# Kernel optimization log

Hardware: AMD Instinct MI355X
Metric: run time of the kernel (lower is better)

Reference implementation:

```python
import jax, jax.numpy as jnp
import numpy as np
import math

NBITS = (1, 2, 4, 8)
S, B, D, H, F = 1024, 8, 1024, 16, 4096
HD = D // H


def _quant(w, nbit):
    """Symmetric uniform weight quantization to `nbit` bits with STE."""
    if nbit == 1:
        q = jnp.sign(w) * jnp.mean(jnp.abs(w))
    else:
        qmax = float(2 ** (nbit - 1) - 1)
        scale = jnp.max(jnp.abs(w)) / qmax
        q = jnp.clip(jnp.round(w / scale), -qmax - 1.0, qmax) * scale
    # straight-through estimator: forward uses q, backward flows through w
    return w + jax.lax.stop_gradient(q - w)


def _layernorm(x, g, b, eps=1e-5):
    m = jnp.mean(x, axis=-1, keepdims=True)
    v = jnp.var(x, axis=-1, keepdims=True)
    return (x - m) * jax.lax.rsqrt(v + eps) * g + b


def _quant_attn(src, w_in, b_in, w_out, b_out, nbit):
    # src: [S,B,D]; w_in: [3D,D]; w_out: [D,D]
    w_in_q = _quant(w_in, nbit)
    w_out_q = _quant(w_out, nbit)
    qkv = jnp.einsum('sbd,ed->sbe', src, w_in_q) + b_in  # [S,B,3D]
    q, k, v = jnp.split(qkv, 3, axis=-1)
    q = q.reshape(S, B, H, HD)
    k = k.reshape(S, B, H, HD)
    v = v.reshape(S, B, H, HD)
    scores = jnp.einsum('sbhd,tbhd->bhst', q, k) * (1.0 / math.sqrt(HD))
    p = jax.nn.softmax(scores, axis=-1)  # [B,H,S,S]
    o = jnp.einsum('bhst,tbhd->sbhd', p, v).reshape(S, B, D)
    return jnp.einsum('sbd,ed->sbe', o, w_out_q) + b_out


def setup_inputs() -> dict:
    key = jax.random.key(0)
    ks = jax.random.split(key, 12)
    sc = 0.02
    return {
        'src': jax.random.normal(ks[0], (S, B, D), jnp.float32),
        'alpha': jax.random.normal(ks[1], (3, 4), jnp.float32),
        'in_proj_w': jax.random.normal(ks[2], (4, 3 * D, D), jnp.float32) * sc,
        'in_proj_b': jnp.zeros((4, 3 * D), jnp.float32),
        'out_proj_w': jax.random.normal(ks[3], (4, D, D), jnp.float32) * sc,
        'out_proj_b': jnp.zeros((4, D), jnp.float32),
        'w1': jax.random.normal(ks[4], (4, F, D), jnp.float32) * sc,
        'b1': jnp.zeros((4, F), jnp.float32),
        'w2': jax.random.normal(ks[5], (4, D, F), jnp.float32) * sc,
        'b2': jnp.zeros((4, D), jnp.float32),
        'g1': jnp.ones((D,), jnp.float32),
        'be1': jnp.zeros((D,), jnp.float32),
        'g2': jnp.ones((D,), jnp.float32),
        'be2': jnp.zeros((D,), jnp.float32),
    }


def reference(src, alpha, in_proj_w, in_proj_b, out_proj_w, out_proj_b,
              w1, b1, w2, b2, g1, be1, g2, be2):
    probs = jax.nn.softmax(alpha, axis=-1)  # [3,4]
    # softmax-weighted mixture of multi-bitwidth attention branches
    src2 = jnp.zeros_like(src)
    for i, nbit in enumerate(NBITS):
        src2 = src2 + probs[0, i] * _quant_attn(
            src, in_proj_w[i], in_proj_b[i], out_proj_w[i], out_proj_b[i], nbit)
    x = _layernorm(src + src2, g1, be1)
    # mixture of quantized linear1 branches, then GELU
    h = jnp.zeros((S, B, F), src.dtype)
    for i, nbit in enumerate(NBITS):
        h = h + probs[1, i] * (jnp.einsum('sbd,fd->sbf', x, _quant(w1[i], nbit)) + b1[i])
    h = jax.nn.gelu(h, approximate=False)
    # mixture of quantized linear2 branches
    y = jnp.zeros_like(x)
    for i, nbit in enumerate(NBITS):
        y = y + probs[2, i] * (jnp.einsum('sbf,df->sbd', h, _quant(w2[i], nbit)) + b2[i])
    return _layernorm(x + y, g2, be2)
```

## Files before the change

kernel.cpp:

```cpp
#include <hip/hip_runtime.h>
#include <hip/hip_bf16.h>

typedef __attribute__((ext_vector_type(8))) unsigned short u16x8;
typedef __attribute__((ext_vector_type(4))) unsigned short u16x4;
typedef __attribute__((ext_vector_type(4))) int            i32x4;
typedef __attribute__((ext_vector_type(8))) __bf16         bf16x8;
typedef __attribute__((ext_vector_type(4))) float          f32x4;

#define SS 1024
#define BB 8
#define DD 1024
#define HH 16
#define HDD 64
#define FF 4096
#define MM 8192

#define GL16(g, l) __builtin_amdgcn_global_load_lds( \
    (__attribute__((address_space(1))) const void*)(g), \
    (__attribute__((address_space(3))) void*)(l), 16, 0, 0)

__device__ __forceinline__ float bf2f(unsigned short u) {
    return __uint_as_float(((unsigned int)u) << 16);
}
__device__ __forceinline__ unsigned short f2bf(float f) {
    return __builtin_bit_cast(unsigned short, (__bf16)f);
}
__device__ __forceinline__ float quantv(float w, float som, float qm) {
    if (qm == 0.f) {
        float sgn = (w > 0.f) ? 1.f : ((w < 0.f) ? -1.f : 0.f);
        return sgn * som;
    }
    if (som == 0.f) return 0.f;
    float q = rintf(w / som);
    q = fminf(fmaxf(q, -qm - 1.f), qm);
    return q * som;
}

__global__ __launch_bounds__(256) void k_stats(const float* __restrict__ w_in, const float* __restrict__ w_out,
                                               const float* __restrict__ w1, const float* __restrict__ w2,
                                               const float* __restrict__ src,
                                               float* __restrict__ pmax, float* __restrict__ psum) {
    const int t = blockIdx.y, blk = blockIdx.x, tid = threadIdx.x;
    const float* base; int n;
    if (t < 4)       { base = w_in  + (size_t)t * 3145728;     n = 3145728; }
    else if (t < 8)  { base = w_out + (size_t)(t-4) * 1048576; n = 1048576; }
    else if (t < 12) { base = w1    + (size_t)(t-8) * 4194304; n = 4194304; }
    else if (t < 16) { base = w2    + (size_t)(t-12) * 4194304; n = 4194304; }
    else             { base = src;                             n = 8388608; }
    const int n4 = n >> 2;
    float vmax = 0.f, vsum = 0.f;
    for (int i = blk * 256 + tid; i < n4; i += 65536) {
        float4 v = reinterpret_cast<const float4*>(base)[i];
        float a0 = fabsf(v.x), a1 = fabsf(v.y), a2 = fabsf(v.z), a3 = fabsf(v.w);
        vmax = fmaxf(vmax, fmaxf(fmaxf(a0, a1), fmaxf(a2, a3)));
        vsum += (a0 + a1) + (a2 + a3);
    }
#pragma unroll
    for (int m = 1; m < 64; m <<= 1) { vmax = fmaxf(vmax, __shfl_xor(vmax, m, 64)); vsum += __shfl_xor(vsum, m, 64); }
    __shared__ float sm[4], su[4];
    const int wave = tid >> 6, lane = tid & 63;
    if (lane == 0) { sm[wave] = vmax; su[wave] = vsum; }
    __syncthreads();
    if (tid == 0) {
        pmax[t * 256 + blk] = fmaxf(fmaxf(sm[0], sm[1]), fmaxf(sm[2], sm[3]));
        psum[t * 256 + blk] = (su[0] + su[1]) + (su[2] + su[3]);
    }
}

__global__ __launch_bounds__(256) void k_params(const float* __restrict__ pmax, const float* __restrict__ psum,
                                                const float* __restrict__ alpha, float* __restrict__ P) {
    __shared__ float rm[256], rs[256];
    const int tid = threadIdx.x;
    for (int t = 0; t < 17; ++t) {
        rm[tid] = pmax[t * 256 + tid];
        rs[tid] = psum[t * 256 + tid];
        __syncthreads();
        for (int s = 128; s > 0; s >>= 1) {
            if (tid < s) { rm[tid] = fmaxf(rm[tid], rm[tid + s]); rs[tid] += rs[tid + s]; }
            __syncthreads();
        }
        if (tid == 0) {
            if (t == 16) {
                P[50] = rm[0] * (1.f / 127.f);
            } else {
                const int nbits[4] = {1, 2, 4, 8};
                const int nb = nbits[t & 3];
                float nsize = (t < 4) ? 3145728.f : ((t < 8) ? 1048576.f : 4194304.f);
                if (nb == 1) { P[16 + 2*t] = rs[0] / nsize; P[17 + 2*t] = 0.f; }
                else { float qm = (float)((1 << (nb - 1)) - 1); P[16 + 2*t] = rm[0] / qm; P[17 + 2*t] = qm; }
            }
        }
        __syncthreads();
    }
    if (tid < 3) {
        float a[4], mx = -1e30f;
#pragma unroll
        for (int i = 0; i < 4; ++i) { a[i] = alpha[tid * 4 + i]; mx = fmaxf(mx, a[i]); }
        float e[4], ssum = 0.f;
#pragma unroll
        for (int i = 0; i < 4; ++i) { e[i] = expf(a[i] - mx); ssum += e[i]; }
#pragma unroll
        for (int i = 0; i < 4; ++i) P[tid * 4 + i] = e[i] / ssum;
    }
}

__global__ __launch_bounds__(256) void k_rmax(const float* __restrict__ part, int n, float* __restrict__ out) {
    const int tid = threadIdx.x;
    float m = 0.f;
    for (int i = tid; i < n; i += 256) m = fmaxf(m, part[i]);
#pragma unroll
    for (int s = 1; s < 64; s <<= 1) m = fmaxf(m, __shfl_xor(m, s, 64));
    __shared__ float sm[4];
    const int wave = tid >> 6, lane = tid & 63;
    if (lane == 0) sm[wave] = m;
    __syncthreads();
    if (tid == 0) *out = fmaxf(fmaxf(sm[0], sm[1]), fmaxf(sm[2], sm[3]));
}

__global__ __launch_bounds__(256) void k_quant8(const float* __restrict__ w, signed char* __restrict__ out,
                                                const float* __restrict__ P, int per_tensor, int tbase, int ntot) {
    int i = blockIdx.x * 256 + threadIdx.x;
    if (i >= ntot) return;
    int t = tbase + i / per_tensor;
    float som = P[16 + 2*t], qm = P[17 + 2*t];
    float v;
    float x = w[i];
    if (qm == 0.f)      v = (x > 0.f) ? 1.f : ((x < 0.f) ? -1.f : 0.f);
    else if (som == 0.f) v = 0.f;
    else                v = fminf(fmaxf(rintf(x / som), -qm - 1.f), qm);
    out[i] = (signed char)(int)v;
}

__global__ __launch_bounds__(256) void k_si8(const float* __restrict__ in, signed char* __restrict__ out,
                                             const float* __restrict__ P, int n4) {
    int i = blockIdx.x * 256 + threadIdx.x;
    if (i >= n4) return;
    const float sa = P[50];
    const float inv = (sa > 0.f) ? 1.f / sa : 0.f;
    float4 v = reinterpret_cast<const float4*>(in)[i];
    char4 o;
    o.x = (signed char)(int)fminf(fmaxf(rintf(v.x * inv), -127.f), 127.f);
    o.y = (signed char)(int)fminf(fmaxf(rintf(v.y * inv), -127.f), 127.f);
    o.z = (signed char)(int)fminf(fmaxf(rintf(v.z * inv), -127.f), 127.f);
    o.w = (signed char)(int)fminf(fmaxf(rintf(v.w * inv), -127.f), 127.f);
    reinterpret_cast<char4*>(out)[i] = o;
}

template <int NE, int MODE>
__global__ __launch_bounds__(256) void k_mixq8(const float* __restrict__ w, signed char* __restrict__ out,
                                               float* __restrict__ sB, const float* __restrict__ P,
                                               int tbase, int prow, size_t sz) {
    const int row = blockIdx.x, tid = threadIdx.x;
    const int L = NE * 256;
    float v[NE];
    float lm = 0.f;
#pragma unroll
    for (int j = 0; j < NE; ++j) {
        int k = j * 256 + tid;
        float acc;
        if (MODE == 0) {
            acc = 0.f;
#pragma unroll
            for (int br = 0; br < 4; ++br) {
                int t = tbase + br;
                acc += P[prow * 4 + br] * quantv(w[(size_t)br * sz + (size_t)row * L + k], P[16 + 2*t], P[17 + 2*t]);
            }
        } else {
            int i = k >> 10, e = k & 1023;
            int t = tbase + i;
            acc = P[i] * quantv(w[(size_t)i * sz + (size_t)row * 1024 + e], P[16 + 2*t], P[17 + 2*t]);
        }
        v[j] = acc;
        lm = fmaxf(lm, fabsf(acc));
    }
#pragma unroll
    for (int m = 1; m < 64; m <<= 1) lm = fmaxf(lm, __shfl_xor(lm, m, 64));
    __shared__ float sm[4];
    const int wave = tid >> 6, lane = tid & 63;
    if (lane == 0) sm[wave] = lm;
    __syncthreads();
    lm = fmaxf(fmaxf(sm[0], sm[1]), fmaxf(sm[2], sm[3]));
    if (tid == 0) sB[row] = lm * (1.f / 127.f);
    const float inv = (lm > 0.f) ? 127.f / lm : 0.f;
#pragma unroll
    for (int j = 0; j < NE; ++j)
        out[(size_t)row * L + j * 256 + tid] =
            (signed char)(int)fminf(fmaxf(rintf(v[j] * inv), -127.f), 127.f);
}

__global__ __launch_bounds__(256) void k_mixb(const float* __restrict__ b, float* __restrict__ out,
                                              const float* __restrict__ P, int prow, int n) {
    int i = blockIdx.x * 256 + threadIdx.x;
    if (i >= n) return;
    float acc = 0.f;
#pragma unroll
    for (int br = 0; br < 4; ++br) acc += P[prow * 4 + br] * b[(size_t)br * n + i];
    out[i] = acc;
}

__global__ __launch_bounds__(256) void k_q8(const unsigned short* __restrict__ in, signed char* __restrict__ out,
                                            const float* __restrict__ amax, int n8) {
    int i = blockIdx.x * 256 + threadIdx.x;
    if (i >= n8) return;
    const float am = *amax;
    const float inv = (am > 0.f) ? 127.f / am : 0.f;
    u16x8 v = reinterpret_cast<const u16x8*>(in)[i];
    union { signed char c[8]; unsigned long long u; } r;
#pragma unroll
    for (int e = 0; e < 8; ++e) {
        float f = bf2f(v[e]) * inv;
        r.c[e] = (signed char)(int)fminf(fmaxf(rintf(f), -127.f), 127.f);
    }
    reinterpret_cast<unsigned long long*>(out)[i] = r.u;
}

__global__ __launch_bounds__(256) void k_gemm_i8(const signed char* __restrict__ A,
                                                 const signed char* __restrict__ Bw,
                                                 unsigned short* __restrict__ C,
                                                 const float* __restrict__ bias,
                                                 const float* __restrict__ P, int tIdx,
                                                 int M, int N, int K, int XM, int XN) {
    const int gx = gridDim.x, gy = gridDim.y;
    const int flat = blockIdx.x + gx * blockIdx.y;
    const int xcd = flat & 7, r = flat >> 3;
    const int nloc = gx / XN, mloc = gy / XM;
    const int cm = xcd / XN, cn = xcd - cm * XN;
    const int by = cm * mloc + r / nloc;
    const int bx = cn * nloc + (r - (r / nloc) * nloc);

    __shared__ signed char As[2][128 * 128];
    __shared__ signed char Bs[2][128 * 128];
    const int tid = threadIdx.x;
    const int m0 = by * 128, n0 = bx * 128;
    const int lane = tid & 63, wave = tid >> 6;
    const int wr = wave >> 1, wc = wave & 1;
    const int lr = lane & 15, lg = lane >> 4;
    const int rsub = lane >> 3;
    const int csub = ((lane & 7) ^ rsub) * 16;
    const size_t aoff = (size_t)(m0 + rsub) * K + csub;
    const size_t boff = (size_t)(n0 + rsub) * K + csub;

    i32x4 acc[4][4];
#pragma unroll
    for (int m = 0; m < 4; ++m)
#pragma unroll
        for (int n = 0; n < 4; ++n) acc[m][n] = (i32x4){0, 0, 0, 0};

    auto stage = [&](int buf, int k0) {
#pragma unroll
        for (int it = 0; it < 4; ++it) {
            const int g = it * 4 + wave;
            GL16(A + aoff + (size_t)g * 8 * K + k0, &As[buf][g * 1024]);
            GL16(Bw + boff + (size_t)g * 8 * K + k0, &Bs[buf][g * 1024]);
        }
    };
    auto compute = [&](int buf) {
#pragma unroll
        for (int kh = 0; kh < 2; ++kh) {
            i32x4 af[4], bfr[4];
#pragma unroll
            for (int m = 0; m < 4; ++m) {
                int row = wr * 64 + m * 16 + lr;
                int cidx = (kh * 4 + lg) ^ (lr & 7);
                af[m] = *reinterpret_cast<const i32x4*>(&As[buf][row * 128 + cidx * 16]);
            }
#pragma unroll
            for (int n = 0; n < 4; ++n) {
                int row = wc * 64 + n * 16 + lr;
                int cidx = (kh * 4 + lg) ^ (lr & 7);
                bfr[n] = *reinterpret_cast<const i32x4*>(&Bs[buf][row * 128 + cidx * 16]);
            }
#pragma unroll
            for (int m = 0; m < 4; ++m)
#pragma unroll
                for (int n = 0; n < 4; ++n)
                    acc[m][n] = __builtin_amdgcn_mfma_i32_16x16x64_i8(
                        af[m], bfr[n], acc[m][n], 0, 0, 0);
        }
    };

    stage(0, 0);
    __syncthreads();
    int cur = 0;
    for (int k0 = 128; k0 < K; k0 += 128) {
        stage(cur ^ 1, k0);
        compute(cur);
        __syncthreads();
        cur ^= 1;
    }
    compute(cur);

    const float sab = P[50] * P[16 + 2 * tIdx];
#pragma unroll
    for (int n = 0; n < 4; ++n) {
        const int col = n0 + wc * 64 + n * 16 + lr;
        const float bv = bias[col];
#pragma unroll
        for (int m = 0; m < 4; ++m) {
#pragma unroll
            for (int j = 0; j < 4; ++j) {
                const int row = m0 + wr * 64 + m * 16 + lg * 4 + j;
                float v = (float)acc[m][n][j] * sab + bv;
                C[(size_t)row * N + col] = f2bf(v);
            }
        }
    }
}

__device__ __forceinline__ void store_out(float* C, size_t idx, float v) { C[idx] = v; }
__device__ __forceinline__ void store_out(unsigned short* C, size_t idx, float v) { C[idx] = f2bf(v); }

template <typename OutT, bool GELU>
__global__ __launch_bounds__(256) void k_gemm_i8s(const signed char* __restrict__ A,
                                                  const signed char* __restrict__ Bw,
                                                  OutT* __restrict__ C,
                                                  const float* __restrict__ bias,
                                                  const float* __restrict__ sB,
                                                  const float* __restrict__ aAm,
                                                  float* __restrict__ oPart,
                                                  int M, int N, int K, int XM, int XN) {
    const int gx = gridDim.x, gy = gridDim.y;
    const int flat = blockIdx.x + gx * blockIdx.y;
    const int xcd = flat & 7, r = flat >> 3;
    const int nloc = gx / XN, mloc = gy / XM;
    const int cm = xcd / XN, cn = xcd - cm * XN;
    const int by = cm * mloc + r / nloc;
    const int bx = cn * nloc + (r - (r / nloc) * nloc);

    __shared__ signed char As[2][128 * 128];
    __shared__ signed char Bs[2][128 * 128];
    __shared__ float smx[4];
    const int tid = threadIdx.x;
    const int m0 = by * 128, n0 = bx * 128;
    const int lane = tid & 63, wave = tid >> 6;
    const int wr = wave >> 1, wc = wave & 1;
    const int lr = lane & 15, lg = lane >> 4;
    const int rsub = lane >> 3;
    const int csub = ((lane & 7) ^ rsub) * 16;
    const size_t aoff = (size_t)(m0 + rsub) * K + csub;
    const size_t boff = (size_t)(n0 + rsub) * K + csub;

    i32x4 acc[4][4];
#pragma unroll
    for (int m = 0; m < 4; ++m)
#pragma unroll
        for (int n = 0; n < 4; ++n) acc[m][n] = (i32x4){0, 0, 0, 0};

    auto stage = [&](int buf, int k0) {
#pragma unroll
        for (int it = 0; it < 4; ++it) {
            const int g = it * 4 + wave;
            GL16(A + aoff + (size_t)g * 8 * K + k0, &As[buf][g * 1024]);
            GL16(Bw + boff + (size_t)g * 8 * K + k0, &Bs[buf][g * 1024]);
        }
    };
    auto compute = [&](int buf) {
#pragma unroll
        for (int kh = 0; kh < 2; ++kh) {
            i32x4 af[4], bfr[4];
#pragma unroll
            for (int m = 0; m < 4; ++m) {
                int row = wr * 64 + m * 16 + lr;
                int cidx = (kh * 4 + lg) ^ (lr & 7);
                af[m] = *reinterpret_cast<const i32x4*>(&As[buf][row * 128 + cidx * 16]);
            }
#pragma unroll
            for (int n = 0; n < 4; ++n) {
                int row = wc * 64 + n * 16 + lr;
                int cidx = (kh * 4 + lg) ^ (lr & 7);
                bfr[n] = *reinterpret_cast<const i32x4*>(&Bs[buf][row * 128 + cidx * 16]);
            }
#pragma unroll
            for (int m = 0; m < 4; ++m)
#pragma unroll
                for (int n = 0; n < 4; ++n)
                    acc[m][n] = __builtin_amdgcn_mfma_i32_16x16x64_i8(
                        af[m], bfr[n], acc[m][n], 0, 0, 0);
        }
    };

    stage(0, 0);
    __syncthreads();
    int cur = 0;
    for (int k0 = 128; k0 < K; k0 += 128) {
        stage(cur ^ 1, k0);
        compute(cur);
        __syncthreads();
        cur ^= 1;
    }
    compute(cur);

    const float sA = (*aAm) * (1.f / 127.f);
    float lm = 0.f;
#pragma unroll
    for (int n = 0; n < 4; ++n) {
        const int col = n0 + wc * 64 + n * 16 + lr;
        const float sc = sA * sB[col];
        const float bv = bias ? bias[col] : 0.f;
#pragma unroll
        for (int m = 0; m < 4; ++m) {
#pragma unroll
            for (int j = 0; j < 4; ++j) {
                const int row = m0 + wr * 64 + m * 16 + lg * 4 + j;
                float v = (float)acc[m][n][j] * sc + bv;
                if (GELU) v = 0.5f * v * (1.f + erff(v * 0.70710678118654752f));
                store_out(C, (size_t)row * N + col, v);
                if (oPart) lm = fmaxf(lm, fabsf(v));
            }
        }
    }
    if (oPart) {
#pragma unroll
        for (int m = 1; m < 64; m <<= 1) lm = fmaxf(lm, __shfl_xor(lm, m, 64));
        if (lane == 0) smx[wave] = lm;
        __syncthreads();
        if (tid == 0) oPart[flat] = fmaxf(fmaxf(smx[0], smx[1]), fmaxf(smx[2], smx[3]));
    }
}

__global__ __launch_bounds__(512) void k_fmfma(const unsigned short* __restrict__ qkvb, int qstride,
                                               unsigned short* __restrict__ outb, int ostride,
                                               float* __restrict__ oPart) {
    __shared__ unsigned short Ks[2][4096];
    __shared__ unsigned short Vt[2][4096];
    __shared__ unsigned short Pl[8 * 16 * 72];
    __shared__ float smx[8];
    const int tid = threadIdx.x;
    const int lane = tid & 63, wave = tid >> 6;
    const int lr = lane & 15, lg = lane >> 4;
    const int f = blockIdx.x;
    const int bh = (f & 7) * 16 + ((f >> 3) & 15);
    const int s0 = (f >> 7) * 256;
    const int b = bh >> 4, hh = bh & 15;
    const int hb = hh * 64;

    u16x8 qf[2][2];
#pragma unroll
    for (int qf2 = 0; qf2 < 2; ++qf2) {
        const size_t qb = (size_t)((s0 + wave * 32 + qf2 * 16 + lr) * 8 + b) * qstride + hb;
#pragma unroll
        for (int ks = 0; ks < 2; ++ks)
            qf[qf2][ks] = *reinterpret_cast<const u16x8*>(qkvb + qb + ks * 32 + lg * 8);
    }
    const int rsub = lane >> 3;
    const int csub = ((lane & 7) ^ rsub) * 8;
    const unsigned short* kS = qkvb + (size_t)(rsub * 8 + b) * qstride + 1024 + hb + csub;

    float m_old[2] = {-1e30f, -1e30f};
    float l_lane[2] = {0.f, 0.f};
    f32x4 oacc[2][4];
#pragma unroll
    for (int qf2 = 0; qf2 < 2; ++qf2)
#pragma unroll
        for (int n = 0; n < 4; ++n) oacc[qf2][n] = (f32x4){0.f, 0.f, 0.f, 0.f};
    unsigned short* myP = Pl + wave * (16 * 72);

    auto stage = [&](int buf, int kt) {
        GL16(kS + (size_t)((kt * 64 + wave * 8) * 8) * qstride, &Ks[buf][wave * 512]);
        const int row = tid >> 3, ch = tid & 7;
        const size_t gb = (size_t)((kt * 64 + row) * 8 + b) * qstride + hb + ch * 8;
        u16x8 vv = *reinterpret_cast<const u16x8*>(qkvb + gb + 2048);
        const int vbase = ((row >> 3) ^ ch) * 8 + (row & 7);
#pragma unroll
        for (int e = 0; e < 8; ++e) Vt[buf][(ch * 8 + e) * 64 + (vbase ^ (e * 8))] = vv[e];
    };

    stage(0, 0);
    __syncthreads();
    int cur = 0;
    for (int kt = 0; kt < 16; ++kt) {
        if (kt < 15) stage(cur ^ 1, kt + 1);
#pragma unroll
        for (int qf2 = 0; qf2 < 2; ++qf2) {
            f32x4 sacc[4];
#pragma unroll
            for (int n = 0; n < 4; ++n) sacc[n] = (f32x4){0.f, 0.f, 0.f, 0.f};
#pragma unroll
            for (int ks = 0; ks < 2; ++ks) {
#pragma unroll
                for (int n = 0; n < 4; ++n) {
                    int row = n * 16 + lr;
                    int cidx = (ks * 4 + lg) ^ (lr & 7);
                    u16x8 kf = *reinterpret_cast<const u16x8*>(&Ks[cur][row * 64 + cidx * 8]);
                    sacc[n] = __builtin_amdgcn_mfma_f32_16x16x32_bf16(
                        __builtin_bit_cast(bf16x8, kf), __builtin_bit_cast(bf16x8, qf[qf2][ks]),
                        sacc[n], 0, 0, 0);
                }
            }
            float pmax = -1e30f;
#pragma unroll
            for (int n = 0; n < 4; ++n)
#pragma unroll
                for (int j = 0; j < 4; ++j) { sacc[n][j] *= 0.125f; pmax = fmaxf(pmax, sacc[n][j]); }
            pmax = fmaxf(pmax, __shfl_xor(pmax, 16, 64));
            pmax = fmaxf(pmax, __shfl_xor(pmax, 32, 64));
            const float m_new = fmaxf(m_old[qf2], pmax);
            const float corr = __expf(m_old[qf2] - m_new);
            float pv[16];
            float psum = 0.f;
#pragma unroll
            for (int n = 0; n < 4; ++n)
#pragma unroll
                for (int j = 0; j < 4; ++j) { float e = __expf(sacc[n][j] - m_new); pv[n * 4 + j] = e; psum += e; }
            l_lane[qf2] = l_lane[qf2] * corr + psum;
            m_old[qf2] = m_new;
#pragma unroll
            for (int n = 0; n < 4; ++n)
#pragma unroll
                for (int t2 = 0; t2 < 2; ++t2) {
                    int key = n * 16 + lg * 4 + t2 * 2;
                    unsigned int pk =
                        (unsigned int)__builtin_bit_cast(unsigned short, (__bf16)pv[n * 4 + t2 * 2]) |
                        ((unsigned int)__builtin_bit_cast(unsigned short, (__bf16)pv[n * 4 + t2 * 2 + 1]) << 16);
                    *reinterpret_cast<unsigned int*>(&myP[lr * 72 + key]) = pk;
                }
#pragma unroll
            for (int j = 0; j < 4; ++j) {
                float cj = __shfl(corr, lg * 4 + j, 64);
#pragma unroll
                for (int n = 0; n < 4; ++n) oacc[qf2][n][j] *= cj;
            }
#pragma unroll
            for (int ks = 0; ks < 2; ++ks) {
                u16x8 pa = *reinterpret_cast<const u16x8*>(&myP[lr * 72 + ks * 32 + lg * 8]);
#pragma unroll
                for (int n = 0; n < 4; ++n) {
                    int d = n * 16 + lr;
                    int kcs = ((ks * 4 + lg) ^ (d >> 3)) ^ (d & 7);
                    u16x8 vf = *reinterpret_cast<const u16x8*>(&Vt[cur][d * 64 + kcs * 8]);
                    oacc[qf2][n] = __builtin_amdgcn_mfma_f32_16x16x32_bf16(
                        __builtin_bit_cast(bf16x8, pa), __builtin_bit_cast(bf16x8, vf),
                        oacc[qf2][n], 0, 0, 0);
                }
            }
        }
        __syncthreads();
        cur ^= 1;
    }
    float lm = 0.f;
#pragma unroll
    for (int qf2 = 0; qf2 < 2; ++qf2) {
        float lsum = l_lane[qf2];
        lsum += __shfl_xor(lsum, 16, 64);
        lsum += __shfl_xor(lsum, 32, 64);
        const float linv = 1.f / lsum;
#pragma unroll
        for (int j = 0; j < 4; ++j) {
            float lj = __shfl(linv, lg * 4 + j, 64);
            const size_t rowb = (size_t)((s0 + wave * 32 + qf2 * 16 + lg * 4 + j) * 8 + b) * ostride + hb;
#pragma unroll
            for (int n = 0; n < 4; ++n) {
                float v = oacc[qf2][n][j] * lj;
                outb[rowb + n * 16 + lr] = f2bf(v);
                lm = fmaxf(lm, fabsf(v));
            }
        }
    }
#pragma unroll
    for (int m = 1; m < 64; m <<= 1) lm = fmaxf(lm, __shfl_xor(lm, m, 64));
    if (lane == 0) smx[wave] = lm;
    __syncthreads();
    if (tid == 0) {
        float t = 0.f;
#pragma unroll
        for (int w = 0; w < 8; ++w) t = fmaxf(t, smx[w]);
        oPart[f] = t;
    }
}

__global__ __launch_bounds__(256) void k_ln(const float* __restrict__ xf, const unsigned short* __restrict__ xb,
                                            const float* __restrict__ r,
                                            const float* __restrict__ g, const float* __restrict__ be,
                                            float* __restrict__ outf, unsigned short* __restrict__ outb,
                                            float* __restrict__ oPart) {
    const int row = blockIdx.x, tid = threadIdx.x;
    const size_t base = (size_t)row * 1024 + tid * 4;
    float x0, x1, x2, x3;
    if (xf) {
        float4 xv = *reinterpret_cast<const float4*>(xf + base);
        x0 = xv.x; x1 = xv.y; x2 = xv.z; x3 = xv.w;
    } else {
        u16x4 xv = *reinterpret_cast<const u16x4*>(xb + base);
        x0 = bf2f(xv[0]); x1 = bf2f(xv[1]); x2 = bf2f(xv[2]); x3 = bf2f(xv[3]);
    }
    float4 rv = *reinterpret_cast<const float4*>(r + base);
    float t0 = x0 + rv.x, t1 = x1 + rv.y, t2 = x2 + rv.z, t3 = x3 + rv.w;
    float s = t0 + t1 + t2 + t3;
    float ss = t0 * t0 + t1 * t1 + t2 * t2 + t3 * t3;
#pragma unroll
    for (int m = 1; m < 64; m <<= 1) { s += __shfl_xor(s, m, 64); ss += __shfl_xor(ss, m, 64); }
    __shared__ float red[8];
    __shared__ float smx[4];
    const int wave = tid >> 6, lane = tid & 63;
    if (lane == 0) { red[wave] = s; red[4 + wave] = ss; }
    __syncthreads();
    s = red[0] + red[1] + red[2] + red[3];
    ss = red[4] + red[5] + red[6] + red[7];
    const float mean = s * (1.f / 1024.f);
    const float var = ss * (1.f / 1024.f) - mean * mean;
    const float rstd = rsqrtf(var + 1e-5f);
    float4 gv = *reinterpret_cast<const float4*>(g + tid * 4);
    float4 bv = *reinterpret_cast<const float4*>(be + tid * 4);
    float o0 = (t0 - mean) * rstd * gv.x + bv.x;
    float o1 = (t1 - mean) * rstd * gv.y + bv.y;
    float o2 = (t2 - mean) * rstd * gv.z + bv.z;
    float o3 = (t3 - mean) * rstd * gv.w + bv.w;
    if (outf) {
        float4 ov = {o0, o1, o2, o3};
        *reinterpret_cast<float4*>(outf + base) = ov;
    }
    if (outb) {
        u16x4 q; q[0] = f2bf(o0); q[1] = f2bf(o1); q[2] = f2bf(o2); q[3] = f2bf(o3);
        *reinterpret_cast<u16x4*>(outb + base) = q;
    }
    if (oPart) {
        float lm = fmaxf(fmaxf(fabsf(o0), fabsf(o1)), fmaxf(fabsf(o2), fabsf(o3)));
#pragma unroll
        for (int m = 1; m < 64; m <<= 1) lm = fmaxf(lm, __shfl_xor(lm, m, 64));
        if (lane == 0) smx[wave] = lm;
        __syncthreads();
        if (tid == 0) oPart[row] = fmaxf(fmaxf(smx[0], smx[1]), fmaxf(smx[2], smx[3]));
    }
}

extern "C" void kernel_launch(void* const* d_in, const int* in_sizes, int n_in,
                              void* d_out, int out_size, void* d_ws, size_t ws_size,
                              hipStream_t stream) {
    const float* src   = (const float*)d_in[0];
    const float* alpha = (const float*)d_in[1];
    const float* w_in  = (const float*)d_in[2];
    const float* b_in  = (const float*)d_in[3];
    const float* w_out = (const float*)d_in[4];
    const float* b_out = (const float*)d_in[5];
    const float* w1    = (const float*)d_in[6];
    const float* b1    = (const float*)d_in[7];
    const float* w2    = (const float*)d_in[8];
    const float* b2    = (const float*)d_in[9];
    const float* g1    = (const float*)d_in[10];
    const float* be1   = (const float*)d_in[11];
    const float* g2    = (const float*)d_in[12];
    const float* be2   = (const float*)d_in[13];

    char* ws = (char*)d_ws;
    size_t off = 0;
    auto alloc = [&](size_t bytes) { size_t r = off; off += (bytes + 255) & ~(size_t)255; return r; };
    float* P              = (float*)(ws + alloc(1024));
    float* amaxv          = (float*)(ws + alloc(256));
    float* flashPart      = (float*)(ws + alloc(8192 * 4));
    float* lnPart         = (float*)(ws + alloc(8192 * 4));
    float* hPart          = (float*)(ws + alloc(2048 * 4));
    float* pmax           = (float*)(ws + alloc(17 * 256 * 4));
    float* psum           = (float*)(ws + alloc(17 * 256 * 4));
    signed char* WinQ8    = (signed char*)(ws + alloc((size_t)4 * 3072 * 1024));
    signed char* WoutC8   = (signed char*)(ws + alloc((size_t)1024 * 4096));
    float* sOut           = (float*)(ws + alloc(1024 * 4));
    signed char* W1m8     = (signed char*)(ws + alloc((size_t)4096 * 1024));
    float* s1             = (float*)(ws + alloc(4096 * 4));
    signed char* W2m8     = (signed char*)(ws + alloc((size_t)1024 * 4096));
    float* s2             = (float*)(ws + alloc(1024 * 4));
    float* b1m            = (float*)(ws + alloc(4096 * 4));
    float* b2m            = (float*)(ws + alloc(1024 * 4));
    float* bOm            = (float*)(ws + alloc(1024 * 4));
    signed char* Si8      = (signed char*)(ws + alloc((size_t)MM * 1024));
    unsigned short* Xbf   = (unsigned short*)(ws + alloc((size_t)MM * 1024 * 2));
    signed char* Xi8      = (signed char*)(ws + alloc((size_t)MM * 1024));
    unsigned short* attnC = (unsigned short*)(ws + alloc((size_t)MM * 4096 * 2));
    unsigned short* qkvB  = (unsigned short*)(ws + alloc((size_t)MM * 3072 * 2));
    signed char* attnC8   = (signed char*)qkvB;
    unsigned short* h     = attnC;
    signed char* h8       = (signed char*)qkvB;
    if (ws_size < off) return;

    float* outF = (float*)d_out;

    k_stats<<<dim3(256, 17), 256, 0, stream>>>(w_in, w_out, w1, w2, src, pmax, psum);
    k_params<<<1, 256, 0, stream>>>(pmax, psum, alpha, P);
    {
        int n = 4 * 3072 * 1024;
        k_quant8<<<(n + 255) / 256, 256, 0, stream>>>(w_in, WinQ8, P, 3072 * 1024, 0, n);
        k_mixq8<16, 1><<<1024, 256, 0, stream>>>(w_out, WoutC8, sOut, P, 4, 0, 1048576);
        k_mixq8<4, 0><<<4096, 256, 0, stream>>>(w1, W1m8, s1, P, 8, 1, 4194304);
        k_mixq8<16, 0><<<1024, 256, 0, stream>>>(w2, W2m8, s2, P, 12, 2, 4194304);
        k_mixb<<<(4096 + 255) / 256, 256, 0, stream>>>(b1, b1m, P, 1, 4096);
        k_mixb<<<(1024 + 255) / 256, 256, 0, stream>>>(b2, b2m, P, 2, 1024);
        k_mixb<<<(1024 + 255) / 256, 256, 0, stream>>>(b_out, bOm, P, 0, 1024);
        k_si8<<<(2097152 + 255) / 256, 256, 0, stream>>>(src, Si8, P, 2097152);
    }
    for (int i = 0; i < 4; ++i) {
        k_gemm_i8<<<dim3(24, 64), 256, 0, stream>>>(
            Si8, WinQ8 + (size_t)i * 3072 * 1024, qkvB, b_in + i * 3072, P, i, MM, 3072, 1024, 1, 8);
        k_fmfma<<<dim3(512), 512, 0, stream>>>(qkvB, 3072, attnC + i * 1024, 4096,
                                               flashPart + i * 512);
    }
    k_rmax<<<1, 256, 0, stream>>>(flashPart, 2048, amaxv + 0);
    k_q8<<<(4194304 + 255) / 256, 256, 0, stream>>>(attnC, attnC8, amaxv + 0, 4194304);
    k_gemm_i8s<float, false><<<dim3(8, 64), 256, 0, stream>>>(
        attnC8, WoutC8, outF, bOm, sOut, amaxv + 0, nullptr, MM, 1024, 4096, 4, 2);
    k_ln<<<MM, 256, 0, stream>>>(src, nullptr, outF, g1, be1, nullptr, Xbf, lnPart);
    k_rmax<<<1, 256, 0, stream>>>(lnPart, 8192, amaxv + 1);
    k_q8<<<(1048576 + 255) / 256, 256, 0, stream>>>(Xbf, Xi8, amaxv + 1, 1048576);
    k_gemm_i8s<unsigned short, true><<<dim3(32, 64), 256, 0, stream>>>(
        Xi8, W1m8, h, b1m, s1, amaxv + 1, hPart, MM, 4096, 1024, 1, 8);
    k_rmax<<<1, 256, 0, stream>>>(hPart, 2048, amaxv + 2);
    k_q8<<<(4194304 + 255) / 256, 256, 0, stream>>>(h, h8, amaxv + 2, 4194304);
    k_gemm_i8s<float, false><<<dim3(8, 64), 256, 0, stream>>>(
        h8, W2m8, outF, b2m, s2, amaxv + 2, nullptr, MM, 1024, 4096, 4, 2);
    k_ln<<<MM, 256, 0, stream>>>(nullptr, Xbf, outF, g2, be2, outF, nullptr, nullptr);
}
```

Baseline: 935.2 us.

## Use LDS transpose reads for V and register-resident P in flash attention

Reworks the attention kernel so V is staged into LDS by async global-to-LDS loads and then read transposed with ds_read_b64_tr_b16. This removes the per-element scalar transpose writes into LDS. The softmax P tile now stays in registers and feeds 16x16x16 MFMAs directly, which drops the per-wave P round trip through LDS. Blocks shrink to 256 threads covering 128 queries with twice as many blocks, and s_setprio hints are added around the MFMA sections. The inline asm with a manual lgkmcnt wait and hardcoded LDS offsets adds fragility around layout correctness.

```diff
diff --git a/kernel.cpp b/kernel.cpp
--- a/kernel.cpp
+++ b/kernel.cpp
@@ -3,9 +3,11 @@
 
 typedef __attribute__((ext_vector_type(8))) unsigned short u16x8;
 typedef __attribute__((ext_vector_type(4))) unsigned short u16x4;
+typedef __attribute__((ext_vector_type(2))) unsigned int   u32x2;
 typedef __attribute__((ext_vector_type(4))) int            i32x4;
 typedef __attribute__((ext_vector_type(8))) __bf16         bf16x8;
 typedef __attribute__((ext_vector_type(4))) float          f32x4;
+typedef __attribute__((address_space(3))) unsigned short   lds_us;
 
 #define SS 1024
 #define BB 8
@@ -18,6 +20,10 @@
 #define GL16(g, l) __builtin_amdgcn_global_load_lds( \
     (__attribute__((address_space(1))) const void*)(g), \
     (__attribute__((address_space(3))) void*)(l), 16, 0, 0)
+
+#define TRV(d, a, o) asm volatile("ds_read_b64_tr_b16 %0, %1 offset:" o : "=v"(d) : "v"(a))
+#define MFMA16(acc, pa, vb) asm volatile("v_mfma_f32_16x16x16_bf16 %0, %1, %2, %0" \
+    : "+v"(acc) : "v"(pa), "v"(vb))
 
 __device__ __forceinline__ float bf2f(unsigned short u) {
     return __uint_as_float(((unsigned int)u) << 16);
@@ -418,51 +424,57 @@
     }
 }
 
-__global__ __launch_bounds__(512) void k_fmfma(const unsigned short* __restrict__ qkvb, int qstride,
+__global__ __launch_bounds__(256) void k_fmfma(const unsigned short* __restrict__ qkvb, int qstride,
                                                unsigned short* __restrict__ outb, int ostride,
                                                float* __restrict__ oPart) {
     __shared__ unsigned short Ks[2][4096];
-    __shared__ unsigned short Vt[2][4096];
-    __shared__ unsigned short Pl[8 * 16 * 72];
-    __shared__ float smx[8];
+    __shared__ unsigned short Vs[2][4096];
+    __shared__ float smx[4];
     const int tid = threadIdx.x;
     const int lane = tid & 63, wave = tid >> 6;
     const int lr = lane & 15, lg = lane >> 4;
     const int f = blockIdx.x;
     const int bh = (f & 7) * 16 + ((f >> 3) & 15);
-    const int s0 = (f >> 7) * 256;
+    const int s0 = (f >> 7) * 128;
     const int b = bh >> 4, hh = bh & 15;
     const int hb = hh * 64;
 
     u16x8 qf[2][2];
 #pragma unroll
-    for (int qf2 = 0; qf2 < 2; ++qf2) {
-        const size_t qb = (size_t)((s0 + wave * 32 + qf2 * 16 + lr) * 8 + b) * qstride + hb;
+    for (int q2 = 0; q2 < 2; ++q2) {
+        const size_t qb = (size_t)((s0 + wave * 32 + q2 * 16 + lr) * 8 + b) * qstride + hb;
 #pragma unroll
         for (int ks = 0; ks < 2; ++ks)
-            qf[qf2][ks] = *reinterpret_cast<const u16x8*>(qkvb + qb + ks * 32 + lg * 8);
-    }
-    const int rsub = lane >> 3;
-    const int csub = ((lane & 7) ^ rsub) * 8;
-    const unsigned short* kS = qkvb + (size_t)(rsub * 8 + b) * qstride + 1024 + hb + csub;
+            qf[q2][ks] = *reinterpret_cast<const u16x8*>(qkvb + qb + ks * 32 + lg * 8);
+    }
+    size_t kOff[2], vOff[2];
+#pragma unroll
+    for (int it = 0; it < 2; ++it) {
+        const int g = it * 256 + tid;
+        const int krow = g >> 3, kchs = g & 7;
+        kOff[it] = (size_t)(krow * 8 + b) * qstride + 1024 + hb + ((kchs ^ (krow & 7)) * 8);
+        const int dblk = (g >> 7) & 3, khi = (g >> 5) & 3, kmid = (g >> 3) & 3, klo = (g >> 1) & 3, dh = g & 1;
+        const int vkey = khi * 16 + kmid * 4 + klo;
+        vOff[it] = (size_t)(vkey * 8 + b) * qstride + 2048 + hb + dblk * 16 + dh * 8;
+    }
+    const lds_us* va0 = (lds_us*)&Vs[0][lg * 64 + lr];
+    const lds_us* va1 = (lds_us*)&Vs[1][lg * 64 + lr];
 
     float m_old[2] = {-1e30f, -1e30f};
     float l_lane[2] = {0.f, 0.f};
     f32x4 oacc[2][4];
 #pragma unroll
-    for (int qf2 = 0; qf2 < 2; ++qf2)
-#pragma unroll
-        for (int n = 0; n < 4; ++n) oacc[qf2][n] = (f32x4){0.f, 0.f, 0.f, 0.f};
-    unsigned short* myP = Pl + wave * (16 * 72);
+    for (int q2 = 0; q2 < 2; ++q2)
+#pragma unroll
+        for (int n = 0; n < 4; ++n) oacc[q2][n] = (f32x4){0.f, 0.f, 0.f, 0.f};
 
     auto stage = [&](int buf, int kt) {
-        GL16(kS + (size_t)((kt * 64 + wave * 8) * 8) * qstride, &Ks[buf][wave * 512]);
-        const int row = tid >> 3, ch = tid & 7;
-        const size_t gb = (size_t)((kt * 64 + row) * 8 + b) * qstride + hb + ch * 8;
-        u16x8 vv = *reinterpret_cast<const u16x8*>(qkvb + gb + 2048);
-        const int vbase = ((row >> 3) ^ ch) * 8 + (row & 7);
-#pragma unroll
-        for (int e = 0; e < 8; ++e) Vt[buf][(ch * 8 + e) * 64 + (vbase ^ (e * 8))] = vv[e];
+        const size_t ktoff = (size_t)kt * 512 * qstride;
+#pragma unroll
+        for (int it = 0; it < 2; ++it) {
+            GL16(qkvb + kOff[it] + ktoff, &Ks[buf][it * 2048 + wave * 512]);
+            GL16(qkvb + vOff[it] + ktoff, &Vs[buf][it * 2048 + wave * 512]);
+        }
     };
 
     stage(0, 0);
@@ -470,11 +482,20 @@
     int cur = 0;
     for (int kt = 0; kt < 16; ++kt) {
         if (kt < 15) stage(cur ^ 1, kt + 1);
-#pragma unroll
-        for (int qf2 = 0; qf2 < 2; ++qf2) {
+        const lds_us* va = cur ? va1 : va0;
+        u32x2 vb[4][4];
+        TRV(vb[0][0], va, "0");    TRV(vb[0][1], va, "2048"); TRV(vb[0][2], va, "4096"); TRV(vb[0][3], va, "6144");
+        TRV(vb[1][0], va, "512");  TRV(vb[1][1], va, "2560"); TRV(vb[1][2], va, "4608"); TRV(vb[1][3], va, "6656");
+        TRV(vb[2][0], va, "1024"); TRV(vb[2][1], va, "3072"); TRV(vb[2][2], va, "5120"); TRV(vb[2][3], va, "7168");
+        TRV(vb[3][0], va, "1536"); TRV(vb[3][1], va, "3584"); TRV(vb[3][2], va, "5632"); TRV(vb[3][3], va, "7680");
+        asm volatile("s_waitcnt lgkmcnt(0)" ::: "memory");
+        __builtin_amdgcn_sched_barrier(0);
+#pragma unroll
+        for (int q2 = 0; q2 < 2; ++q2) {
             f32x4 sacc[4];
 #pragma unroll
             for (int n = 0; n < 4; ++n) sacc[n] = (f32x4){0.f, 0.f, 0.f, 0.f};
+            __builtin_amdgcn_s_setprio(1);
 #pragma unroll
             for (int ks = 0; ks < 2; ++ks) {
 #pragma unroll
@@ -483,10 +504,11 @@
                     int cidx = (ks * 4 + lg) ^ (lr & 7);
                     u16x8 kf = *reinterpret_cast<const u16x8*>(&Ks[cur][row * 64 + cidx * 8]);
                     sacc[n] = __builtin_amdgcn_mfma_f32_16x16x32_bf16(
-                        __builtin_bit_cast(bf16x8, kf), __builtin_bit_cast(bf16x8, qf[qf2][ks]),
+                        __builtin_bit_cast(bf16x8, kf), __builtin_bit_cast(bf16x8, qf[q2][ks]),
                         sacc[n], 0, 0, 0);
                 }
             }
+            __builtin_amdgcn_s_setprio(0);
             float pmax = -1e30f;
 #pragma unroll
             for (int n = 0; n < 4; ++n)
@@ -494,63 +516,53 @@
                 for (int j = 0; j < 4; ++j) { sacc[n][j] *= 0.125f; pmax = fmaxf(pmax, sacc[n][j]); }
             pmax = fmaxf(pmax, __shfl_xor(pmax, 16, 64));
             pmax = fmaxf(pmax, __shfl_xor(pmax, 32, 64));
-            const float m_new = fmaxf(m_old[qf2], pmax);
-            const float corr = __expf(m_old[qf2] - m_new);
+            const float m_new = fmaxf(m_old[q2], pmax);
+            const float corr = __expf(m_old[q2] - m_new);
             float pv[16];
             float psum = 0.f;
 #pragma unroll
             for (int n = 0; n < 4; ++n)
 #pragma unroll
                 for (int j = 0; j < 4; ++j) { float e = __expf(sacc[n][j] - m_new); pv[n * 4 + j] = e; psum += e; }
-            l_lane[qf2] = l_lane[qf2] * corr + psum;
-            m_old[qf2] = m_new;
-#pragma unroll
-            for (int n = 0; n < 4; ++n)
-#pragma unroll
-                for (int t2 = 0; t2 < 2; ++t2) {
-                    int key = n * 16 + lg * 4 + t2 * 2;
-                    unsigned int pk =
-                        (unsigned int)__builtin_bit_cast(unsigned short, (__bf16)pv[n * 4 + t2 * 2]) |
-                        ((unsigned int)__builtin_bit_cast(unsigned short, (__bf16)pv[n * 4 + t2 * 2 + 1]) << 16);
-                    *reinterpret_cast<unsigned int*>(&myP[lr * 72 + key]) = pk;
-                }
+            l_lane[q2] = l_lane[q2] * corr + psum;
+            m_old[q2] = m_new;
+            u32x2 pa[4];
+#pragma unroll
+            for (int n = 0; n < 4; ++n) {
+                pa[n][0] = (unsigned)f2bf(pv[n * 4 + 0]) | ((unsigned)f2bf(pv[n * 4 + 1]) << 16);
+                pa[n][1] = (unsigned)f2bf(pv[n * 4 + 2]) | ((unsigned)f2bf(pv[n * 4 + 3]) << 16);
+            }
 #pragma unroll
             for (int j = 0; j < 4; ++j) {
                 float cj = __shfl(corr, lg * 4 + j, 64);
 #pragma unroll
-                for (int n = 0; n < 4; ++n) oacc[qf2][n][j] *= cj;
-            }
-#pragma unroll
-            for (int ks = 0; ks < 2; ++ks) {
-                u16x8 pa = *reinterpret_cast<const u16x8*>(&myP[lr * 72 + ks * 32 + lg * 8]);
-#pragma unroll
-                for (int n = 0; n < 4; ++n) {
-                    int d = n * 16 + lr;
-                    int kcs = ((ks * 4 + lg) ^ (d >> 3)) ^ (d & 7);
-                    u16x8 vf = *reinterpret_cast<const u16x8*>(&Vt[cur][d * 64 + kcs * 8]);
-                    oacc[qf2][n] = __builtin_amdgcn_mfma_f32_16x16x32_bf16(
-                        __builtin_bit_cast(bf16x8, pa), __builtin_bit_cast(bf16x8, vf),
-                        oacc[qf2][n], 0, 0, 0);
-                }
-            }
+                for (int n = 0; n < 4; ++n) oacc[q2][n][j] *= cj;
+            }
+            __builtin_amdgcn_s_setprio(1);
+#pragma unroll
+            for (int n = 0; n < 4; ++n)
+#pragma unroll
+                for (int dblk = 0; dblk < 4; ++dblk)
+                    MFMA16(oacc[q2][dblk], pa[n], vb[n][dblk]);
+            __builtin_amdgcn_s_setprio(0);
         }
         __syncthreads();
         cur ^= 1;
     }
     float lm = 0.f;
 #pragma unroll
-    for (int qf2 = 0; qf2 < 2; ++qf2) {
-        float lsum = l_lane[qf2];
+    for (int q2 = 0; q2 < 2; ++q2) {
+        float lsum = l_lane[q2];
         lsum += __shfl_xor(lsum, 16, 64);
         lsum += __shfl_xor(lsum, 32, 64);
         const float linv = 1.f / lsum;
 #pragma unroll
         for (int j = 0; j < 4; ++j) {
             float lj = __shfl(linv, lg * 4 + j, 64);
-            const size_t rowb = (size_t)((s0 + wave * 32 + qf2 * 16 + lg * 4 + j) * 8 + b) * ostride + hb;
+            const size_t rowb = (size_t)((s0 + wave * 32 + q2 * 16 + lg * 4 + j) * 8 + b) * ostride + hb;
 #pragma unroll
             for (int n = 0; n < 4; ++n) {
-                float v = oacc[qf2][n][j] * lj;
+                float v = oacc[q2][n][j] * lj;
                 outb[rowb + n * 16 + lr] = f2bf(v);
                 lm = fmaxf(lm, fabsf(v));
             }
@@ -560,12 +572,7 @@
     for (int m = 1; m < 64; m <<= 1) lm = fmaxf(lm, __shfl_xor(lm, m, 64));
     if (lane == 0) smx[wave] = lm;
     __syncthreads();
-    if (tid == 0) {
-        float t = 0.f;
-#pragma unroll
-        for (int w = 0; w < 8; ++w) t = fmaxf(t, smx[w]);
-        oPart[f] = t;
-    }
+    if (tid == 0) oPart[f] = fmaxf(fmaxf(smx[0], smx[1]), fmaxf(smx[2], smx[3]));
 }
 
 __global__ __launch_bounds__(256) void k_ln(const float* __restrict__ xf, const unsigned short* __restrict__ xb,
@@ -646,7 +653,7 @@
     auto alloc = [&](size_t bytes) { size_t r = off; off += (bytes + 255) & ~(size_t)255; return r; };
     float* P              = (float*)(ws + alloc(1024));
     float* amaxv          = (float*)(ws + alloc(256));
-    float* flashPart      = (float*)(ws + alloc(8192 * 4));
+    float* flashPart      = (float*)(ws + alloc(4096 * 4));
     float* lnPart         = (float*)(ws + alloc(8192 * 4));
     float* hPart          = (float*)(ws + alloc(2048 * 4));
     float* pmax           = (float*)(ws + alloc(17 * 256 * 4));
@@ -689,10 +696,10 @@
     for (int i = 0; i < 4; ++i) {
         k_gemm_i8<<<dim3(24, 64), 256, 0, stream>>>(
             Si8, WinQ8 + (size_t)i * 3072 * 1024, qkvB, b_in + i * 3072, P, i, MM, 3072, 1024, 1, 8);
-        k_fmfma<<<dim3(512), 512, 0, stream>>>(qkvB, 3072, attnC + i * 1024, 4096,
-                                               flashPart + i * 512);
-    }
-    k_rmax<<<1, 256, 0, stream>>>(flashPart, 2048, amaxv + 0);
+        k_fmfma<<<dim3(1024), 256, 0, stream>>>(qkvB, 3072, attnC + i * 1024, 4096,
+                                                flashPart + i * 1024);
+    }
+    k_rmax<<<1, 256, 0, stream>>>(flashPart, 4096, amaxv + 0);
     k_q8<<<(4194304 + 255) / 256, 256, 0, stream>>>(attnC, attnC8, amaxv + 0, 4194304);
     k_gemm_i8s<float, false><<<dim3(8, 64), 256, 0, stream>>>(
         attnC8, WoutC8, outF, bOm, sOut, amaxv + 0, nullptr, MM, 1024, 4096, 4, 2);
```

Measured after the change: 888.0 us. -5.1%, faster.
